# Kernel optimization log

Measured on AMD Instinct MI355X. Metric: run time of the kernel, lower is better.

## Reference

```python
import jax, jax.numpy as jnp
import numpy as np

VOCAB, S, D, H, DH, L, W1S, DFF = 50265, 4096, 768, 12, 64, 2, 256, 3072


def layer_norm(x, g, b, eps=1e-5):
    m = jnp.mean(x, axis=-1, keepdims=True)
    v = jnp.mean((x - m) ** 2, axis=-1, keepdims=True)
    return (x - m) * jax.lax.rsqrt(v + eps) * g + b


def sliding_global_attn(q, k, v, att, w=W1S):
    # q,k,v: [B,H,S,Dh]; att: [B,S] float (1 real / 0 pad). Longformer-style
    # sliding window (one-sided w) + global attention on token 0.
    B, nh, S_, Dh = q.shape
    nc = S_ // w
    q = q * (Dh ** -0.5)
    k_pad = jnp.pad(k, ((0, 0), (0, 0), (w, w), (0, 0)))
    v_pad = jnp.pad(v, ((0, 0), (0, 0), (w, w), (0, 0)))
    idx = jnp.arange(nc)[:, None] * w + jnp.arange(3 * w)[None, :]  # [nc,3w] into padded axis
    k_band = k_pad[:, :, idx]  # [B,H,nc,3w,Dh]
    v_band = v_pad[:, :, idx]
    qc = q.reshape(B, nh, nc, w, Dh)
    s_loc = jnp.einsum('bhcqd,bhckd->bhcqk', qc, k_band)  # [B,H,nc,w,3w]
    rel = jnp.arange(3 * w)[None, :] - jnp.arange(w)[:, None]  # [w,3w]
    band_ok = (rel >= 0) & (rel <= 2 * w)
    key_abs = idx - w  # [nc,3w] absolute key positions
    in_seq = (key_abs >= 0) & (key_abs < S_) & (key_abs != 0)  # token 0 handled by global column
    key_real = att[:, jnp.clip(key_abs, 0, S_ - 1)] > 0  # [B,nc,3w]
    valid = band_ok[None, None, None] & in_seq[None, None, :, None, :] & key_real[:, None, :, None, :]
    s_loc = jnp.where(valid, s_loc, -1e9)
    s_g = jnp.einsum('bhcqd,bhd->bhcq', qc, k[:, :, 0])  # global key column
    p = jax.nn.softmax(jnp.concatenate([s_g[..., None], s_loc], axis=-1), axis=-1)
    out = (jnp.einsum('bhcq,bhd->bhcqd', p[..., 0], v[:, :, 0])
           + jnp.einsum('bhcqk,bhckd->bhcqd', p[..., 1:], v_band)).reshape(B, nh, S_, Dh)
    # global token 0 attends to everything
    s0 = jnp.where(att[:, None, :] > 0, jnp.einsum('bhd,bhsd->bhs', q[:, :, 0], k), -1e9)
    out0 = jnp.einsum('bhs,bhsd->bhd', jax.nn.softmax(s0, axis=-1), v)
    return out.at[:, :, 0].set(out0)


def setup_inputs() -> dict:
    key = jax.random.key(0)
    ks = jax.random.split(key, 16)
    sc = 0.02
    inp = {
        'input_ids': jax.random.randint(ks[0], (2, S), 0, VOCAB, dtype=jnp.int64)
        if jax.config.jax_enable_x64 else jax.random.randint(ks[0], (2, S), 0, VOCAB, dtype=jnp.int32),
        'attention_mask': jnp.ones((2, S), dtype=jnp.int32),
        'word_emb': sc * jax.random.normal(ks[1], (VOCAB, D), jnp.float32),
        'pos_emb': sc * jax.random.normal(ks[2], (S, D), jnp.float32),
        'emb_ln_g': jnp.ones((D,), jnp.float32), 'emb_ln_b': jnp.zeros((D,), jnp.float32),
        'Wq': sc * jax.random.normal(ks[3], (L, D, D), jnp.float32), 'bq': jnp.zeros((L, D), jnp.float32),
        'Wk': sc * jax.random.normal(ks[4], (L, D, D), jnp.float32), 'bk': jnp.zeros((L, D), jnp.float32),
        'Wv': sc * jax.random.normal(ks[5], (L, D, D), jnp.float32), 'bv': jnp.zeros((L, D), jnp.float32),
        'Wo': sc * jax.random.normal(ks[6], (L, D, D), jnp.float32), 'bo': jnp.zeros((L, D), jnp.float32),
        'ln1_g': jnp.ones((L, D), jnp.float32), 'ln1_b': jnp.zeros((L, D), jnp.float32),
        'Wf1': sc * jax.random.normal(ks[7], (L, D, DFF), jnp.float32), 'bf1': jnp.zeros((L, DFF), jnp.float32),
        'Wf2': sc * jax.random.normal(ks[8], (L, DFF, D), jnp.float32), 'bf2': jnp.zeros((L, D), jnp.float32),
        'ln2_g': jnp.ones((L, D), jnp.float32), 'ln2_b': jnp.zeros((L, D), jnp.float32),
        'Wh1': sc * jax.random.normal(ks[9], (D, 256), jnp.float32), 'bh1': jnp.zeros((256,), jnp.float32),
        'Wh2': sc * jax.random.normal(ks[10], (256, 14), jnp.float32), 'bh2': jnp.zeros((14,), jnp.float32),
    }
    return inp


def reference(input_ids, attention_mask, word_emb, pos_emb, emb_ln_g, emb_ln_b,
              Wq, bq, Wk, bk, Wv, bv, Wo, bo, ln1_g, ln1_b,
              Wf1, bf1, Wf2, bf2, ln2_g, ln2_b, Wh1, bh1, Wh2, bh2):
    B, S_ = input_ids.shape
    att = attention_mask.astype(jnp.float32)
    x = word_emb[input_ids] + pos_emb[None, :S_, :]
    x = layer_norm(x, emb_ln_g, emb_ln_b)
    for l in range(L):
        def heads(w, b):
            return (x @ w + b).reshape(B, S_, H, DH).transpose(0, 2, 1, 3)
        q = heads(Wq[l], bq[l]); k = heads(Wk[l], bk[l]); v = heads(Wv[l], bv[l])
        a = sliding_global_attn(q, k, v, att)
        a = a.transpose(0, 2, 1, 3).reshape(B, S_, D) @ Wo[l] + bo[l]
        x = layer_norm(x + a, ln1_g[l], ln1_b[l])
        f = jax.nn.gelu(x @ Wf1[l] + bf1[l]) @ Wf2[l] + bf2[l]
        x = layer_norm(x + f, ln2_g[l], ln2_b[l])
    # masked mean pool
    m = att[..., None]
    pooled = jnp.sum(x * m, axis=1) / jnp.clip(jnp.sum(m, axis=1), 1e-9)
    h = jax.nn.relu(pooled @ Wh1 + bh1)
    return jax.nn.sigmoid(h @ Wh2 + bh2) * 4.0
```

## Files before the change

kernel.cpp:

```cpp
#include <hip/hip_runtime.h>
#include <hip/hip_bf16.h>
#include <math.h>

#define S_LEN 4096
#define D_MODEL 768
#define NHEAD 12
#define DH 64
#define NLAYER 2
#define DFF 3072
#define BATCH 2
#define QSTR 2304

typedef __attribute__((ext_vector_type(8))) __bf16 bf16x8;
typedef __attribute__((ext_vector_type(4))) float f32x4;

__device__ __forceinline__ unsigned short f2bf_bits(float f) {
  unsigned int u = __float_as_uint(f);
  unsigned int r = (u + 0x7fffu + ((u >> 16) & 1u)) >> 16;
  return (unsigned short)r;
}

__device__ __forceinline__ float bf2f(unsigned short u) {
  return __uint_as_float(((unsigned int)u) << 16);
}

__device__ __forceinline__ unsigned int cvtpk_bf16(float lo, float hi) {
  unsigned int d;
  asm("v_cvt_pk_bf16_f32 %0, %1, %2" : "=v"(d) : "v"(lo), "v"(hi));
  return d;
}

#define ASYNC_COPY16(gsrc, ldst)                                       \
  __builtin_amdgcn_global_load_lds(                                    \
      (const __attribute__((address_space(1))) void*)(gsrc),           \
      (__attribute__((address_space(3))) void*)(ldst), 16, 0, 0)

#define MFMA_BF16(a, b, c) __builtin_amdgcn_mfma_f32_16x16x32_bf16(a, b, c, 0, 0, 0)

__device__ __forceinline__ float blk_sum256(float v, float* lds) {
#pragma unroll
  for (int off = 32; off > 0; off >>= 1) v += __shfl_down(v, off, 64);
  __syncthreads();
  if ((threadIdx.x & 63) == 0) lds[threadIdx.x >> 6] = v;
  __syncthreads();
  return lds[0] + lds[1] + lds[2] + lds[3];
}

__global__ __launch_bounds__(256) void wconv_kernel(
    const float* __restrict__ Wq, const float* __restrict__ Wk,
    const float* __restrict__ Wv, const float* __restrict__ Wo,
    const float* __restrict__ Wf1, const float* __restrict__ Wf2,
    unsigned short* __restrict__ Wbf) {
  int id = blockIdx.x;
  const float* src;
  unsigned short* dst;
  int K, N, t;
  if (id < 4608) {
    int m = id / 576;
    t = id % 576;
    int layer = m >> 2, which = m & 3;
    const float* s = (which == 0) ? Wq : (which == 1) ? Wk : (which == 2) ? Wv : Wo;
    src = s + (size_t)layer * 589824;
    dst = Wbf + (size_t)layer * 7077888 + (size_t)which * 589824;
    K = 768; N = 768;
  } else if (id < 9216) {
    int j = id - 4608;
    int layer = j / 2304;
    t = j % 2304;
    src = Wf1 + (size_t)layer * 2359296;
    dst = Wbf + (size_t)layer * 7077888 + 2359296;
    K = 768; N = 3072;
  } else {
    int j = id - 9216;
    int layer = j / 2304;
    t = j % 2304;
    src = Wf2 + (size_t)layer * 2359296;
    dst = Wbf + (size_t)layer * 7077888 + 4718592;
    K = 3072; N = 768;
  }
  int tiles_n = N >> 5;
  int tk = t / tiles_n, tn = t % tiles_n;
  __shared__ float tile[32][33];
  int c = threadIdx.x & 31, r0 = threadIdx.x >> 5;
#pragma unroll
  for (int p = 0; p < 4; ++p) {
    int r = r0 + p * 8;
    tile[r][c] = src[(size_t)(tk * 32 + r) * N + tn * 32 + c];
  }
  __syncthreads();
#pragma unroll
  for (int p = 0; p < 4; ++p) {
    int r = r0 + p * 8;
    dst[(size_t)(tn * 32 + r) * K + tk * 32 + c] = f2bf_bits(tile[c][r]);
  }
}

__global__ __launch_bounds__(256) void embed_ln_kernel(
    const int* __restrict__ ids, const float* __restrict__ wemb,
    const float* __restrict__ pemb, const float* __restrict__ g,
    const float* __restrict__ b, float* __restrict__ X,
    unsigned short* __restrict__ Xb) {
  int row = blockIdx.x;
  int s = row % S_LEN;
  int id = ids[row];
  const float* we = wemb + (size_t)id * D_MODEL;
  const float* pe = pemb + (size_t)s * D_MODEL;
  int t = threadIdx.x;
  __shared__ float lds[4];
  float v0 = we[t] + pe[t];
  float v1 = we[t + 256] + pe[t + 256];
  float v2 = we[t + 512] + pe[t + 512];
  float mean = blk_sum256(v0 + v1 + v2, lds) * (1.f / 768.f);
  float d0 = v0 - mean, d1 = v1 - mean, d2 = v2 - mean;
  float var = blk_sum256(d0 * d0 + d1 * d1 + d2 * d2, lds) * (1.f / 768.f);
  float rs = rsqrtf(var + 1e-5f);
  float o0 = d0 * rs * g[t] + b[t];
  float o1 = d1 * rs * g[t + 256] + b[t + 256];
  float o2 = d2 * rs * g[t + 512] + b[t + 512];
  float* xp = X + (size_t)row * D_MODEL;
  xp[t] = o0; xp[t + 256] = o1; xp[t + 512] = o2;
  unsigned short* xb = Xb + (size_t)row * D_MODEL;
  xb[t] = f2bf_bits(o0); xb[t + 256] = f2bf_bits(o1); xb[t + 512] = f2bf_bits(o2);
}

__global__ __launch_bounds__(256) void ln_kernel(
    const float* __restrict__ T, const float* __restrict__ g,
    const float* __restrict__ b, float* __restrict__ X,
    unsigned short* __restrict__ Xb) {
  int row = blockIdx.x;
  const float* tp = T + (size_t)row * D_MODEL;
  int t = threadIdx.x;
  __shared__ float lds[4];
  float v0 = tp[t], v1 = tp[t + 256], v2 = tp[t + 512];
  float mean = blk_sum256(v0 + v1 + v2, lds) * (1.f / 768.f);
  float d0 = v0 - mean, d1 = v1 - mean, d2 = v2 - mean;
  float var = blk_sum256(d0 * d0 + d1 * d1 + d2 * d2, lds) * (1.f / 768.f);
  float rs = rsqrtf(var + 1e-5f);
  float o0 = d0 * rs * g[t] + b[t];
  float o1 = d1 * rs * g[t + 256] + b[t + 256];
  float o2 = d2 * rs * g[t + 512] + b[t + 512];
  float* xp = X + (size_t)row * D_MODEL;
  xp[t] = o0; xp[t + 256] = o1; xp[t + 512] = o2;
  unsigned short* xb = Xb + (size_t)row * D_MODEL;
  xb[t] = f2bf_bits(o0); xb[t + 256] = f2bf_bits(o1); xb[t + 512] = f2bf_bits(o2);
}

template <int MODE>
__global__ __launch_bounds__(256) void gemm_bf16(
    const unsigned short* __restrict__ A, const unsigned short* __restrict__ Bt,
    const float* __restrict__ bias0, const float* __restrict__ bias1,
    const float* __restrict__ bias2, const float* __restrict__ Res,
    void* __restrict__ Cout, int M, int N, int K) {
  __shared__ unsigned short Abuf[3][128 * 32];
  __shared__ unsigned short Bbuf[3][128 * 32];
  const int tid = threadIdx.x;
  const int lane = tid & 63, w = tid >> 6;
  const int wm = w >> 1, wn = w & 1;

  const int nbx = gridDim.x;
  const int nwg = nbx * gridDim.y;
  const int orig = blockIdx.y * nbx + blockIdx.x;
  const int wgid = (orig & 7) * (nwg >> 3) + (orig >> 3);
  const int m0 = (wgid / nbx) * 128, n0 = (wgid % nbx) * 128;

  f32x4 acc[4][4];
#pragma unroll
  for (int i = 0; i < 4; ++i)
#pragma unroll
    for (int j = 0; j < 4; ++j) acc[i][j] = (f32x4){0.f, 0.f, 0.f, 0.f};

  const int s0 = w * 64 + lane, s1 = s0 + 256;
  const int r0 = s0 >> 2, c0 = (s0 & 3) ^ (r0 & 3);
  const int r1 = s1 >> 2, c1 = (s1 & 3) ^ (r1 & 3);
  const unsigned short* gA0 = A + (size_t)(m0 + r0) * K + c0 * 8;
  const unsigned short* gA1 = A + (size_t)(m0 + r1) * K + c1 * 8;
  const unsigned short* gB0 = Bt + (size_t)(n0 + r0) * K + c0 * 8;
  const unsigned short* gB1 = Bt + (size_t)(n0 + r1) * K + c1 * 8;
  const int dA0 = (w * 64) * 8, dA1 = (256 + w * 64) * 8;

  const int frow = lane & 15, kgrp = lane >> 4;
  int aoff[4], boff[4];
#pragma unroll
  for (int i = 0; i < 4; ++i) {
    int ra = wm * 64 + i * 16 + frow;
    int rb = wn * 64 + i * 16 + frow;
    aoff[i] = ra * 32 + ((kgrp ^ (ra & 3)) * 8);
    boff[i] = rb * 32 + ((kgrp ^ (rb & 3)) * 8);
  }

#define STAGE(bsel)                                                       \
  {                                                                       \
    ASYNC_COPY16(gA0, &Abuf[bsel][dA0]);                                  \
    ASYNC_COPY16(gA1, &Abuf[bsel][dA1]);                                  \
    ASYNC_COPY16(gB0, &Bbuf[bsel][dA0]);                                  \
    ASYNC_COPY16(gB1, &Bbuf[bsel][dA1]);                                  \
    gA0 += 32; gA1 += 32; gB0 += 32; gB1 += 32;                           \
  }

  const int nk = K >> 5;
  STAGE(0);
  if (nk > 1) STAGE(1);
  asm volatile("s_waitcnt vmcnt(4)" ::: "memory");
  __builtin_amdgcn_s_barrier();
  __builtin_amdgcn_sched_barrier(0);

  int cur = 0;
  for (int kt = 0; kt < nk; ++kt) {
    if (kt + 2 < nk) {
      int nxt = cur + 2;
      if (nxt >= 3) nxt -= 3;
      STAGE(nxt);
    }
    bf16x8 av[4], bv[4];
#pragma unroll
    for (int i = 0; i < 4; ++i) av[i] = *(const bf16x8*)(&Abuf[cur][aoff[i]]);
#pragma unroll
    for (int j = 0; j < 4; ++j) bv[j] = *(const bf16x8*)(&Bbuf[cur][boff[j]]);
#pragma unroll
    for (int i = 0; i < 4; ++i)
#pragma unroll
      for (int j = 0; j < 4; ++j)
        acc[i][j] = MFMA_BF16(av[i], bv[j], acc[i][j]);
    if (kt + 1 < nk) {
      if (kt + 2 < nk)
        asm volatile("s_waitcnt vmcnt(4)" ::: "memory");
      else
        asm volatile("s_waitcnt vmcnt(0)" ::: "memory");
      __builtin_amdgcn_s_barrier();
      __builtin_amdgcn_sched_barrier(0);
    }
    cur = (cur == 2) ? 0 : cur + 1;
  }
#undef STAGE

#pragma unroll
  for (int i = 0; i < 4; ++i) {
#pragma unroll
    for (int j = 0; j < 4; ++j) {
      int grb = m0 + wm * 64 + i * 16 + (lane >> 4) * 4;
      int gc = n0 + wn * 64 + j * 16 + (lane & 15);
      float bsv;
      if (MODE == 4)
        bsv = (gc < 768) ? bias0[gc] : (gc < 1536) ? bias1[gc - 768] : bias2[gc - 1536];
      else
        bsv = bias0[gc];
#pragma unroll
      for (int r = 0; r < 4; ++r) {
        int gr = grb + r;
        float v = acc[i][j][r] + bsv;
        if (MODE == 1) {
          float x = v;
          float th = tanhf(0.7978845608028654f * (x + 0.044715f * x * x * x));
          v = 0.5f * x * (1.f + th);
        }
        if (MODE == 4 && gc < 768) v *= 0.125f;
        if (MODE == 2) v += Res[(size_t)gr * N + gc];
        if (MODE == 1 || MODE == 4)
          ((unsigned short*)Cout)[(size_t)gr * N + gc] = f2bf_bits(v);
        else
          ((float*)Cout)[(size_t)gr * N + gc] = v;
      }
    }
  }
}

__global__ __launch_bounds__(256) void vtrans_kernel(
    const unsigned short* __restrict__ Vsrc, unsigned short* __restrict__ Vt) {
  int kb = blockIdx.x, h = blockIdx.y, b = blockIdx.z;
  int k0 = kb * 64;
  const size_t bs = (size_t)b * S_LEN;
  const size_t bh = (size_t)(b * NHEAD + h);
  __shared__ unsigned short tile[64][72];
  int tid = threadIdx.x;
#pragma unroll
  for (int p = 0; p < 2; ++p) {
    int idx = p * 256 + tid;
    int key = idx >> 3, ch = idx & 7;
    bf16x8 v = *(const bf16x8*)(Vsrc + (bs + k0 + key) * QSTR + h * DH + ch * 8);
    *(bf16x8*)&tile[key][ch * 8] = v;
  }
  __syncthreads();
#pragma unroll
  for (int p = 0; p < 2; ++p) {
    int idx = p * 256 + tid;
    int d = idx >> 3, kc = idx & 7;
    unsigned int w0 = tile[kc * 8 + 0][d] | ((unsigned int)tile[kc * 8 + 1][d] << 16);
    unsigned int w1 = tile[kc * 8 + 2][d] | ((unsigned int)tile[kc * 8 + 3][d] << 16);
    unsigned int w2 = tile[kc * 8 + 4][d] | ((unsigned int)tile[kc * 8 + 5][d] << 16);
    unsigned int w3 = tile[kc * 8 + 6][d] | ((unsigned int)tile[kc * 8 + 7][d] << 16);
    uint4 out = make_uint4(w0, w1, w2, w3);
    *(uint4*)(Vt + (bh * 64 + d) * S_LEN + k0 + kc * 8) = out;
  }
}

__global__ __launch_bounds__(512) void band_attn_kernel(
    const unsigned short* __restrict__ Qg, const unsigned short* __restrict__ Kgb,
    const unsigned short* __restrict__ Vgb, const unsigned short* __restrict__ Vt,
    const int* __restrict__ att, unsigned short* __restrict__ Aout) {
  const int c = blockIdx.x, h = blockIdx.y, b = blockIdx.z;
  const int tid = threadIdx.x;
  const int lane = tid & 63, wq = tid >> 6;
  const int g = lane >> 4, cl = lane & 15;
  const size_t bs = (size_t)b * S_LEN;
  const size_t bh = (size_t)(b * NHEAD + h);

  __shared__ __align__(16) char smem[18944];

  if (c == 16) {
    float* sc = (float*)smem;
    float* q0 = sc + S_LEN;
    float* red = q0 + 64;
    float* part = red + 8;
    if (tid < 64) q0[tid] = bf2f(Qg[bs * QSTR + h * DH + tid]);
    __syncthreads();
    float lmax = -1e30f;
    for (int s = tid; s < S_LEN; s += 512) {
      const unsigned short* kp = Kgb + (bs + s) * QSTR + h * DH;
      float acc = 0.f;
#pragma unroll
      for (int cc = 0; cc < 8; ++cc) {
        uint4 u = *(const uint4*)(kp + cc * 8);
        const unsigned int* uu = (const unsigned int*)&u;
#pragma unroll
        for (int w2 = 0; w2 < 4; ++w2) {
          unsigned int x = uu[w2];
          acc += q0[cc * 8 + w2 * 2] * __uint_as_float(x << 16);
          acc += q0[cc * 8 + w2 * 2 + 1] * __uint_as_float(x & 0xffff0000u);
        }
      }
      acc = (att[b * S_LEN + s] > 0) ? acc : -1e9f;
      sc[s] = acc;
      lmax = fmaxf(lmax, acc);
    }
#pragma unroll
    for (int off = 32; off > 0; off >>= 1) lmax = fmaxf(lmax, __shfl_down(lmax, off, 64));
    __syncthreads();
    if (lane == 0) red[wq] = lmax;
    __syncthreads();
    float M = red[0];
#pragma unroll
    for (int i = 1; i < 8; ++i) M = fmaxf(M, red[i]);
    float lsum = 0.f;
    for (int s = tid; s < S_LEN; s += 512) {
      float p = __expf(sc[s] - M);
      sc[s] = p;
      lsum += p;
    }
#pragma unroll
    for (int off = 32; off > 0; off >>= 1) lsum += __shfl_down(lsum, off, 64);
    __syncthreads();
    if (lane == 0) red[wq] = lsum;
    __syncthreads();
    float L = red[0];
#pragma unroll
    for (int i = 1; i < 8; ++i) L += red[i];
    int d = tid & 63, chunk = tid >> 6;
    float acc2 = 0.f;
    for (int s = chunk * 512; s < (chunk + 1) * 512; ++s)
      acc2 += sc[s] * bf2f(Vgb[(bs + s) * QSTR + h * DH + d]);
    part[chunk * 64 + d] = acc2;
    __syncthreads();
    if (tid < 64) {
      float v = 0.f;
#pragma unroll
      for (int i = 0; i < 8; ++i) v += part[i * 64 + tid];
      Aout[bs * D_MODEL + h * DH + tid] = f2bf_bits(v / L);
    }
    return;
  }

  unsigned short* Klds = (unsigned short*)smem;
  unsigned short* Vlds = Klds + 64 * 64;
  float* kmask = (float*)(Vlds + 64 * 64);

  bf16x8 qf[2][2];
#pragma unroll
  for (int qt = 0; qt < 2; ++qt)
#pragma unroll
    for (int ks = 0; ks < 2; ++ks)
      qf[qt][ks] = *(const bf16x8*)(Qg + (bs + c * 256 + wq * 32 + qt * 16 + cl) * QSTR +
                                    h * DH + ks * 32 + g * 8);

  float mrun[2], lrun[2];
  f32x4 oacc[2][4];
#pragma unroll
  for (int qt = 0; qt < 2; ++qt) {
    float sg = 0.f;
#pragma unroll
    for (int ks = 0; ks < 2; ++ks) {
      bf16x8 k0 = *(const bf16x8*)(Kgb + bs * QSTR + h * DH + ks * 32 + g * 8);
#pragma unroll
      for (int j = 0; j < 8; ++j) sg += (float)qf[qt][ks][j] * (float)k0[j];
    }
    sg += __shfl_xor(sg, 16, 64);
    sg += __shfl_xor(sg, 32, 64);
    mrun[qt] = sg;
    lrun[qt] = 1.f;
  }
#pragma unroll
  for (int dt = 0; dt < 4; ++dt) {
    float v0d = bf2f(Vgb[bs * QSTR + h * DH + dt * 16 + cl]);
    f32x4 vv = {v0d, v0d, v0d, v0d};
    oacc[0][dt] = vv;
    oacc[1][dt] = vv;
  }

  const int jlo = wq * 32, jhi = wq * 32 + 543;

  for (int t = 0; t < 12; ++t) {
    int kabs0 = c * 256 - 256 + t * 64;
    if (kabs0 < 0 || kabs0 >= S_LEN) continue;
    __syncthreads();
    {
      int key = tid >> 3, ch = tid & 7;
      bf16x8 kv = *(const bf16x8*)(Kgb + (bs + kabs0 + key) * QSTR + h * DH + ch * 8);
      *(bf16x8*)(Klds + key * 64 + ((ch ^ (key & 7)) * 8)) = kv;
      bf16x8 vv = *(const bf16x8*)(Vt + (bh * 64 + key) * S_LEN + kabs0 + ch * 8);
      *(bf16x8*)(Vlds + key * 64 + ((ch ^ (key & 7)) * 8)) = vv;
      if (tid < 64) {
        int ka = kabs0 + tid;
        kmask[tid] = (ka >= 1 && att[b * S_LEN + ka] > 0) ? 0.f : -1e9f;
      }
    }
    __syncthreads();
    if (t * 64 + 63 < jlo || t * 64 > jhi) continue;

    f32x4 accs[4][2];
#pragma unroll
    for (int kt = 0; kt < 4; ++kt) {
      accs[kt][0] = (f32x4){0.f, 0.f, 0.f, 0.f};
      accs[kt][1] = (f32x4){0.f, 0.f, 0.f, 0.f};
    }
#pragma unroll
    for (int ks = 0; ks < 2; ++ks) {
      bf16x8 kf[4];
#pragma unroll
      for (int kt = 0; kt < 4; ++kt) {
        int key = kt * 16 + cl;
        kf[kt] = *(const bf16x8*)(Klds + key * 64 + (((ks * 4 + g) ^ (key & 7)) * 8));
      }
#pragma unroll
      for (int kt = 0; kt < 4; ++kt) {
        accs[kt][0] = MFMA_BF16(kf[kt], qf[0][ks], accs[kt][0]);
        accs[kt][1] = MFMA_BF16(kf[kt], qf[1][ks], accs[kt][1]);
      }
    }

#pragma unroll
    for (int qt = 0; qt < 2; ++qt) {
      int iq = wq * 32 + qt * 16 + cl;
      int relbase = t * 64 - iq;
      float pvv[4][4];
      float tmax = -1e30f;
#pragma unroll
      for (int kt = 0; kt < 4; ++kt)
#pragma unroll
        for (int r = 0; r < 4; ++r) {
          int key = kt * 16 + g * 4 + r;
          int rel = relbase + key;
          float x = accs[kt][qt][r] + kmask[key];
          x = (rel >= 0 && rel <= 512) ? x : -1e9f;
          pvv[kt][r] = x;
          tmax = fmaxf(tmax, x);
        }
      tmax = fmaxf(tmax, __shfl_xor(tmax, 16, 64));
      tmax = fmaxf(tmax, __shfl_xor(tmax, 32, 64));
      float mnew = fmaxf(mrun[qt], tmax);
      float scale = __expf(mrun[qt] - mnew);
      mrun[qt] = mnew;
      float psum = 0.f;
#pragma unroll
      for (int kt = 0; kt < 4; ++kt)
#pragma unroll
        for (int r = 0; r < 4; ++r) {
          float p = __expf(pvv[kt][r] - mnew);
          pvv[kt][r] = p;
          psum += p;
        }
      psum += __shfl_xor(psum, 16, 64);
      psum += __shfl_xor(psum, 32, 64);
      lrun[qt] = lrun[qt] * scale + psum;
      float scr[4];
#pragma unroll
      for (int r = 0; r < 4; ++r) scr[r] = __shfl(scale, g * 4 + r, 64);
#pragma unroll
      for (int dt = 0; dt < 4; ++dt) {
        oacc[qt][dt][0] *= scr[0];
        oacc[qt][dt][1] *= scr[1];
        oacc[qt][dt][2] *= scr[2];
        oacc[qt][dt][3] *= scr[3];
      }
#pragma unroll
      for (int ks = 0; ks < 2; ++ks) {
        unsigned int E0D0 = cvtpk_bf16(pvv[ks * 2][0], pvv[ks * 2][1]);
        unsigned int E0D1 = cvtpk_bf16(pvv[ks * 2][2], pvv[ks * 2][3]);
        unsigned int E1D0 = cvtpk_bf16(pvv[ks * 2 + 1][0], pvv[ks * 2 + 1][1]);
        unsigned int E1D1 = cvtpk_bf16(pvv[ks * 2 + 1][2], pvv[ks * 2 + 1][3]);
        int src0 = ((lane >> 4) & 1) * 32 + cl;
        int src1 = src0 + 16;
        unsigned int a0 = (unsigned int)__shfl((int)E0D0, src0, 64);
        unsigned int a1 = (unsigned int)__shfl((int)E0D1, src0, 64);
        unsigned int a2 = (unsigned int)__shfl((int)E0D0, src1, 64);
        unsigned int a3 = (unsigned int)__shfl((int)E0D1, src1, 64);
        unsigned int b0 = (unsigned int)__shfl((int)E1D0, src0, 64);
        unsigned int b1 = (unsigned int)__shfl((int)E1D1, src0, 64);
        unsigned int b2 = (unsigned int)__shfl((int)E1D0, src1, 64);
        unsigned int b3 = (unsigned int)__shfl((int)E1D1, src1, 64);
        bool hi = lane >= 32;
        union { unsigned int u[4]; bf16x8 v; } af;
        af.u[0] = hi ? b0 : a0;
        af.u[1] = hi ? b1 : a1;
        af.u[2] = hi ? b2 : a2;
        af.u[3] = hi ? b3 : a3;
#pragma unroll
        for (int dt = 0; dt < 4; ++dt) {
          int d = dt * 16 + cl;
          bf16x8 vf = *(const bf16x8*)(Vlds + d * 64 + (((ks * 4 + g) ^ (d & 7)) * 8));
          oacc[qt][dt] = MFMA_BF16(af.v, vf, oacc[qt][dt]);
        }
      }
    }
  }

#pragma unroll
  for (int qt = 0; qt < 2; ++qt) {
    float lr[4];
#pragma unroll
    for (int r = 0; r < 4; ++r) lr[r] = 1.f / __shfl(lrun[qt], g * 4 + r, 64);
#pragma unroll
    for (int dt = 0; dt < 4; ++dt)
#pragma unroll
      for (int r = 0; r < 4; ++r) {
        int row = c * 256 + wq * 32 + qt * 16 + g * 4 + r;
        if (row != 0)
          Aout[(bs + row) * D_MODEL + h * DH + dt * 16 + cl] =
              f2bf_bits(oacc[qt][dt][r] * lr[r]);
      }
  }
}

__global__ __launch_bounds__(256) void pool1_kernel(
    const float* __restrict__ X, const int* __restrict__ att,
    float* __restrict__ ppart) {
  int sb = blockIdx.x, b = blockIdx.y, t = threadIdx.x;
  float a0 = 0.f, a1 = 0.f, a2 = 0.f;
  for (int s = sb * 256; s < sb * 256 + 256; ++s) {
    float a = (float)att[b * S_LEN + s];
    const float* xp = X + ((size_t)b * S_LEN + s) * D_MODEL;
    a0 += xp[t] * a; a1 += xp[t + 256] * a; a2 += xp[t + 512] * a;
  }
  float* pp = ppart + ((size_t)b * 16 + sb) * D_MODEL;
  pp[t] = a0; pp[t + 256] = a1; pp[t + 512] = a2;
}

__global__ __launch_bounds__(256) void pool2_kernel(
    const float* __restrict__ ppart, const int* __restrict__ att,
    float* __restrict__ pooled) {
  int b = blockIdx.x, t = threadIdx.x;
  float a0 = 0.f, a1 = 0.f, a2 = 0.f;
  for (int sb = 0; sb < 16; ++sb) {
    const float* pp = ppart + ((size_t)b * 16 + sb) * D_MODEL;
    a0 += pp[t]; a1 += pp[t + 256]; a2 += pp[t + 512];
  }
  float cnt = 0.f;
  for (int s = 0; s < S_LEN; ++s) cnt += (float)att[b * S_LEN + s];
  cnt = fmaxf(cnt, 1e-9f);
  pooled[b * D_MODEL + t]       = a0 / cnt;
  pooled[b * D_MODEL + t + 256] = a1 / cnt;
  pooled[b * D_MODEL + t + 512] = a2 / cnt;
}

__global__ __launch_bounds__(256) void head_kernel(
    const float* __restrict__ pooled, const float* __restrict__ Wh1,
    const float* __restrict__ bh1, const float* __restrict__ Wh2,
    const float* __restrict__ bh2, float* __restrict__ out) {
  __shared__ float hbuf[2][256];
  int t = threadIdx.x;
  for (int b = 0; b < 2; ++b) {
    float acc = bh1[t];
    for (int d = 0; d < D_MODEL; ++d) acc += pooled[b * D_MODEL + d] * Wh1[d * 256 + t];
    hbuf[b][t] = fmaxf(acc, 0.f);
  }
  __syncthreads();
  if (t < 28) {
    int b = t / 14, j = t % 14;
    float acc = bh2[j];
    for (int i = 0; i < 256; ++i) acc += hbuf[b][i] * Wh2[i * 14 + j];
    out[t] = 4.f / (1.f + __expf(-acc));
  }
}

extern "C" void kernel_launch(void* const* d_in, const int* in_sizes, int n_in,
                              void* d_out, int out_size, void* d_ws,
                              size_t ws_size, hipStream_t stream) {
  const int* ids    = (const int*)d_in[0];
  const int* att    = (const int*)d_in[1];
  const float* wemb = (const float*)d_in[2];
  const float* pemb = (const float*)d_in[3];
  const float* elng = (const float*)d_in[4];
  const float* elnb = (const float*)d_in[5];
  const float* Wq   = (const float*)d_in[6];
  const float* bq   = (const float*)d_in[7];
  const float* Wk   = (const float*)d_in[8];
  const float* bk   = (const float*)d_in[9];
  const float* Wv   = (const float*)d_in[10];
  const float* bv   = (const float*)d_in[11];
  const float* Wo   = (const float*)d_in[12];
  const float* bo   = (const float*)d_in[13];
  const float* ln1g = (const float*)d_in[14];
  const float* ln1b = (const float*)d_in[15];
  const float* Wf1  = (const float*)d_in[16];
  const float* bf1  = (const float*)d_in[17];
  const float* Wf2  = (const float*)d_in[18];
  const float* bf2  = (const float*)d_in[19];
  const float* ln2g = (const float*)d_in[20];
  const float* ln2b = (const float*)d_in[21];
  const float* Wh1  = (const float*)d_in[22];
  const float* bh1  = (const float*)d_in[23];
  const float* Wh2  = (const float*)d_in[24];
  const float* bh2  = (const float*)d_in[25];

  const int M = BATCH * S_LEN;
  float* ws = (float*)d_ws;
  float* X  = ws;
  float* T  = ws + 6291456;
  unsigned short* QKV = (unsigned short*)(ws + 12582912);
  unsigned short* Vt  = (unsigned short*)(ws + 22020096);
  unsigned short* FFbf = QKV;
  unsigned short* Abbf = (unsigned short*)(ws + 23592960);
  unsigned short* Xbf  = (unsigned short*)(ws + 26738688);
  unsigned short* Wbf  = (unsigned short*)(ws + 29884416);
  float* pooled = ws + 36962304;
  float* ppart  = ws + 36963840;

  wconv_kernel<<<13824, 256, 0, stream>>>(Wq, Wk, Wv, Wo, Wf1, Wf2, Wbf);
  embed_ln_kernel<<<M, 256, 0, stream>>>(ids, wemb, pemb, elng, elnb, X, Xbf);

  for (int l = 0; l < NLAYER; ++l) {
    const unsigned short* wqkv = Wbf + (size_t)l * 7077888;
    const unsigned short* wot  = wqkv + 1769472;
    const unsigned short* wf1t = wqkv + 2359296;
    const unsigned short* wf2t = wqkv + 4718592;

    gemm_bf16<4><<<dim3(18, 64), 256, 0, stream>>>(
        Xbf, wqkv, bq + l * D_MODEL, bk + l * D_MODEL, bv + l * D_MODEL,
        nullptr, QKV, M, QSTR, 768);

    vtrans_kernel<<<dim3(64, NHEAD, BATCH), 256, 0, stream>>>(QKV + 1536, Vt);
    band_attn_kernel<<<dim3(17, NHEAD, BATCH), 512, 0, stream>>>(
        QKV, QKV + 768, QKV + 1536, Vt, att, Abbf);

    gemm_bf16<2><<<dim3(6, 64), 256, 0, stream>>>(
        Abbf, wot, bo + l * D_MODEL, nullptr, nullptr, X, T, M, 768, 768);
    ln_kernel<<<M, 256, 0, stream>>>(T, ln1g + l * D_MODEL, ln1b + l * D_MODEL, X, Xbf);

    gemm_bf16<1><<<dim3(24, 64), 256, 0, stream>>>(
        Xbf, wf1t, bf1 + l * DFF, nullptr, nullptr, nullptr, FFbf, M, DFF, 768);
    gemm_bf16<2><<<dim3(6, 64), 256, 0, stream>>>(
        FFbf, wf2t, bf2 + l * D_MODEL, nullptr, nullptr, X, T, M, 768, DFF);
    ln_kernel<<<M, 256, 0, stream>>>(T, ln2g + l * D_MODEL, ln2b + l * D_MODEL, X, Xbf);
  }

  pool1_kernel<<<dim3(16, BATCH), 256, 0, stream>>>(X, att, ppart);
  pool2_kernel<<<BATCH, 256, 0, stream>>>(ppart, att, pooled);
  head_kernel<<<1, 256, 0, stream>>>(pooled, Wh1, bh1, Wh2, bh2, (float*)d_out);
}
```

Measured before the change: 876.1 us.

## Add 256x256-tile 8-wave GEMM with interleaved LDS staging for QKV and FFN1

Adds a new bf16 GEMM kernel with 256x256 output tiles, 512 threads, BK=64, XOR-swizzled LDS, double buffering, and the A/B prefetch interleaved between four MFMA quadrant phases with setprio. The QKV projection and FFN up-projection with GELU now use it, to raise arithmetic intensity and overlap global loads with MFMA work. GELU switches from tanhf to an exp-based formula. The old GEMM is reduced to the fp32 residual mode. The larger tiles give fewer workgroups (288 and 384), which risks underfilling the GPU's CUs and lowering occupancy.

```diff
diff --git a/kernel.cpp b/kernel.cpp
--- a/kernel.cpp
+++ b/kernel.cpp
@@ -28,6 +28,13 @@
   unsigned int d;
   asm("v_cvt_pk_bf16_f32 %0, %1, %2" : "=v"(d) : "v"(lo), "v"(hi));
   return d;
+}
+
+__device__ __forceinline__ float gelu_fast(float x) {
+  float u = 0.7978845608028654f * (x + 0.044715f * x * x * x);
+  float t2 = fminf(fmaxf(2.f * u, -18.f), 18.f);
+  float e = __expf(t2);
+  return 0.5f * x * (1.f + (e - 1.f) / (e + 1.f));
 }
 
 #define ASYNC_COPY16(gsrc, ldst)                                       \
@@ -146,10 +153,185 @@
 }
 
 template <int MODE>
+__global__ __launch_bounds__(512, 2) void gemm8p(
+    const unsigned short* __restrict__ A, const unsigned short* __restrict__ Bt,
+    const float* __restrict__ bias0, const float* __restrict__ bias1,
+    const float* __restrict__ bias2, unsigned short* __restrict__ Cout,
+    int M, int N, int K) {
+  __shared__ unsigned short Abuf[2][256 * 64];
+  __shared__ unsigned short Bbuf[2][256 * 64];
+  const int tid = threadIdx.x;
+  const int lane = tid & 63, w = tid >> 6;
+  const int wm = w >> 2, wn = w & 3;
+  const int cl = lane & 15, kgrp = lane >> 4;
+
+  const int nbx = gridDim.x;
+  const int nwg = nbx * gridDim.y;
+  const int orig = blockIdx.y * nbx + blockIdx.x;
+  const int wgid = (orig & 7) * (nwg >> 3) + (orig >> 3);
+  const int m0 = (wgid / nbx) * 256, n0 = (wgid % nbx) * 256;
+
+  f32x4 acc[8][4];
+#pragma unroll
+  for (int i = 0; i < 8; ++i)
+#pragma unroll
+    for (int j = 0; j < 4; ++j) acc[i][j] = (f32x4){0.f, 0.f, 0.f, 0.f};
+
+  const int lrow = lane >> 3, lch = (lane & 7) ^ lrow;
+  const unsigned short* gA[4];
+  const unsigned short* gB[4];
+  int dstA[4], dstB[4];
+#pragma unroll
+  for (int j = 0; j < 4; ++j) {
+    int arl = wm * 128 + wn * 32 + j * 8;
+    gA[j] = A + (size_t)(m0 + arl + lrow) * K + lch * 8;
+    dstA[j] = arl * 64;
+    int brl = (wn >> 1) * 128 + (wm * 2 + (wn & 1)) * 32 + j * 8;
+    gB[j] = Bt + (size_t)(n0 + brl + lrow) * K + lch * 8;
+    dstB[j] = brl * 64;
+  }
+
+#define STAGE_A(pp)                                                   \
+  {                                                                   \
+    _Pragma("unroll") for (int j = 0; j < 4; ++j) {                   \
+      ASYNC_COPY16(gA[j], &Abuf[pp][dstA[j]]);                        \
+      gA[j] += 64;                                                    \
+    }                                                                 \
+  }
+#define STAGE_B(pp)                                                   \
+  {                                                                   \
+    _Pragma("unroll") for (int j = 0; j < 4; ++j) {                   \
+      ASYNC_COPY16(gB[j], &Bbuf[pp][dstB[j]]);                        \
+      gB[j] += 64;                                                    \
+    }                                                                 \
+  }
+
+  const int nk = K >> 6;
+  STAGE_A(0);
+  STAGE_B(0);
+  asm volatile("s_waitcnt vmcnt(0)" ::: "memory");
+  __builtin_amdgcn_s_barrier();
+  __builtin_amdgcn_sched_barrier(0);
+
+  bf16x8 a[4][2], b0[2][2], b1[2][2];
+  for (int t = 0; t < nk; ++t) {
+    const int p = t & 1;
+    const bool pre = (t + 1 < nk);
+
+#pragma unroll
+    for (int i = 0; i < 4; ++i)
+#pragma unroll
+      for (int ks = 0; ks < 2; ++ks) {
+        int row = wm * 128 + i * 16 + cl;
+        a[i][ks] = *(const bf16x8*)(&Abuf[p][row * 64 + ((((ks << 2) | kgrp) ^ (cl & 7)) << 3)]);
+      }
+#pragma unroll
+    for (int n = 0; n < 2; ++n)
+#pragma unroll
+      for (int ks = 0; ks < 2; ++ks) {
+        int row = wn * 64 + n * 16 + cl;
+        b0[n][ks] = *(const bf16x8*)(&Bbuf[p][row * 64 + ((((ks << 2) | kgrp) ^ (cl & 7)) << 3)]);
+      }
+    if (pre) STAGE_A(p ^ 1);
+    __builtin_amdgcn_s_barrier();
+    asm volatile("s_waitcnt lgkmcnt(0)" ::: "memory");
+    __builtin_amdgcn_sched_barrier(0);
+    __builtin_amdgcn_s_setprio(1);
+#pragma unroll
+    for (int i = 0; i < 4; ++i)
+#pragma unroll
+      for (int n = 0; n < 2; ++n)
+#pragma unroll
+        for (int ks = 0; ks < 2; ++ks)
+          acc[i][n] = MFMA_BF16(a[i][ks], b0[n][ks], acc[i][n]);
+    __builtin_amdgcn_s_setprio(0);
+    __builtin_amdgcn_s_barrier();
+
+#pragma unroll
+    for (int n = 0; n < 2; ++n)
+#pragma unroll
+      for (int ks = 0; ks < 2; ++ks) {
+        int row = wn * 64 + 32 + n * 16 + cl;
+        b1[n][ks] = *(const bf16x8*)(&Bbuf[p][row * 64 + ((((ks << 2) | kgrp) ^ (cl & 7)) << 3)]);
+      }
+    if (pre) STAGE_B(p ^ 1);
+    __builtin_amdgcn_s_barrier();
+    asm volatile("s_waitcnt lgkmcnt(0)" ::: "memory");
+    __builtin_amdgcn_sched_barrier(0);
+    __builtin_amdgcn_s_setprio(1);
+#pragma unroll
+    for (int i = 0; i < 4; ++i)
+#pragma unroll
+      for (int n = 0; n < 2; ++n)
+#pragma unroll
+        for (int ks = 0; ks < 2; ++ks)
+          acc[i][2 + n] = MFMA_BF16(a[i][ks], b1[n][ks], acc[i][2 + n]);
+    __builtin_amdgcn_s_setprio(0);
+    __builtin_amdgcn_s_barrier();
+
+#pragma unroll
+    for (int i = 0; i < 4; ++i)
+#pragma unroll
+      for (int ks = 0; ks < 2; ++ks) {
+        int row = wm * 128 + 64 + i * 16 + cl;
+        a[i][ks] = *(const bf16x8*)(&Abuf[p][row * 64 + ((((ks << 2) | kgrp) ^ (cl & 7)) << 3)]);
+      }
+    __builtin_amdgcn_s_barrier();
+    asm volatile("s_waitcnt lgkmcnt(0)" ::: "memory");
+    __builtin_amdgcn_sched_barrier(0);
+    __builtin_amdgcn_s_setprio(1);
+#pragma unroll
+    for (int i = 0; i < 4; ++i)
+#pragma unroll
+      for (int n = 0; n < 2; ++n)
+#pragma unroll
+        for (int ks = 0; ks < 2; ++ks)
+          acc[4 + i][n] = MFMA_BF16(a[i][ks], b0[n][ks], acc[4 + i][n]);
+    __builtin_amdgcn_s_setprio(0);
+    __builtin_amdgcn_s_barrier();
+
+    __builtin_amdgcn_s_setprio(1);
+#pragma unroll
+    for (int i = 0; i < 4; ++i)
+#pragma unroll
+      for (int n = 0; n < 2; ++n)
+#pragma unroll
+        for (int ks = 0; ks < 2; ++ks)
+          acc[4 + i][2 + n] = MFMA_BF16(a[i][ks], b1[n][ks], acc[4 + i][2 + n]);
+    __builtin_amdgcn_s_setprio(0);
+    if (pre) asm volatile("s_waitcnt vmcnt(0)" ::: "memory");
+    __builtin_amdgcn_s_barrier();
+    __builtin_amdgcn_sched_barrier(0);
+  }
+#undef STAGE_A
+#undef STAGE_B
+
+#pragma unroll
+  for (int mi = 0; mi < 8; ++mi) {
+#pragma unroll
+    for (int ni = 0; ni < 4; ++ni) {
+      int gr0 = m0 + wm * 128 + mi * 16 + kgrp * 4;
+      int gc = n0 + wn * 64 + ni * 16 + cl;
+      float bsv;
+      if (MODE == 4)
+        bsv = (gc < 768) ? bias0[gc] : (gc < 1536) ? bias1[gc - 768] : bias2[gc - 1536];
+      else
+        bsv = bias0[gc];
+#pragma unroll
+      for (int r = 0; r < 4; ++r) {
+        float v = acc[mi][ni][r] + bsv;
+        if (MODE == 1) v = gelu_fast(v);
+        if (MODE == 4 && gc < 768) v *= 0.125f;
+        Cout[(size_t)(gr0 + r) * N + gc] = f2bf_bits(v);
+      }
+    }
+  }
+}
+
+template <int MODE>
 __global__ __launch_bounds__(256) void gemm_bf16(
     const unsigned short* __restrict__ A, const unsigned short* __restrict__ Bt,
-    const float* __restrict__ bias0, const float* __restrict__ bias1,
-    const float* __restrict__ bias2, const float* __restrict__ Res,
+    const float* __restrict__ bias0, const float* __restrict__ Res,
     void* __restrict__ Cout, int M, int N, int K) {
   __shared__ unsigned short Abuf[3][128 * 32];
   __shared__ unsigned short Bbuf[3][128 * 32];
@@ -239,26 +421,13 @@
     for (int j = 0; j < 4; ++j) {
       int grb = m0 + wm * 64 + i * 16 + (lane >> 4) * 4;
       int gc = n0 + wn * 64 + j * 16 + (lane & 15);
-      float bsv;
-      if (MODE == 4)
-        bsv = (gc < 768) ? bias0[gc] : (gc < 1536) ? bias1[gc - 768] : bias2[gc - 1536];
-      else
-        bsv = bias0[gc];
+      float bsv = bias0[gc];
 #pragma unroll
       for (int r = 0; r < 4; ++r) {
         int gr = grb + r;
         float v = acc[i][j][r] + bsv;
-        if (MODE == 1) {
-          float x = v;
-          float th = tanhf(0.7978845608028654f * (x + 0.044715f * x * x * x));
-          v = 0.5f * x * (1.f + th);
-        }
-        if (MODE == 4 && gc < 768) v *= 0.125f;
         if (MODE == 2) v += Res[(size_t)gr * N + gc];
-        if (MODE == 1 || MODE == 4)
-          ((unsigned short*)Cout)[(size_t)gr * N + gc] = f2bf_bits(v);
-        else
-          ((float*)Cout)[(size_t)gr * N + gc] = v;
+        ((float*)Cout)[(size_t)gr * N + gc] = v;
       }
     }
   }
@@ -642,22 +811,22 @@
     const unsigned short* wf1t = wqkv + 2359296;
     const unsigned short* wf2t = wqkv + 4718592;
 
-    gemm_bf16<4><<<dim3(18, 64), 256, 0, stream>>>(
+    gemm8p<4><<<dim3(9, 32), 512, 0, stream>>>(
         Xbf, wqkv, bq + l * D_MODEL, bk + l * D_MODEL, bv + l * D_MODEL,
-        nullptr, QKV, M, QSTR, 768);
+        QKV, M, QSTR, 768);
 
     vtrans_kernel<<<dim3(64, NHEAD, BATCH), 256, 0, stream>>>(QKV + 1536, Vt);
     band_attn_kernel<<<dim3(17, NHEAD, BATCH), 512, 0, stream>>>(
         QKV, QKV + 768, QKV + 1536, Vt, att, Abbf);
 
     gemm_bf16<2><<<dim3(6, 64), 256, 0, stream>>>(
-        Abbf, wot, bo + l * D_MODEL, nullptr, nullptr, X, T, M, 768, 768);
+        Abbf, wot, bo + l * D_MODEL, X, T, M, 768, 768);
     ln_kernel<<<M, 256, 0, stream>>>(T, ln1g + l * D_MODEL, ln1b + l * D_MODEL, X, Xbf);
 
-    gemm_bf16<1><<<dim3(24, 64), 256, 0, stream>>>(
-        Xbf, wf1t, bf1 + l * DFF, nullptr, nullptr, nullptr, FFbf, M, DFF, 768);
+    gemm8p<1><<<dim3(12, 32), 512, 0, stream>>>(
+        Xbf, wf1t, bf1 + l * DFF, nullptr, nullptr, FFbf, M, DFF, 768);
     gemm_bf16<2><<<dim3(6, 64), 256, 0, stream>>>(
-        FFbf, wf2t, bf2 + l * D_MODEL, nullptr, nullptr, X, T, M, 768, DFF);
+        FFbf, wf2t, bf2 + l * D_MODEL, X, T, M, 768, DFF);
     ln_kernel<<<M, 256, 0, stream>>>(T, ln2g + l * D_MODEL, ln2b + l * D_MODEL, X, Xbf);
   }
 
```

Measured after the change: 905.9 us. +3.4%, slower.
